# Optimization experiments

Hardware: AMD Instinct MI355X
Metric: run time of the kernel (lower is better)

## Reference

```python
import jax, jax.numpy as jnp
import numpy as np
from jax import lax

DIM = 512          # model dim
L = 32             # img_size
N = L * L          # tokens
H = 4              # heads
C = DIM // 4       # channels per Res2Net scale
D = C // H         # per-head dim = 32 (== dim_head)
B = 8
SCALE = 32 ** -0.5  # dim_head ** -0.5
EPS = 1e-5


def setup_inputs() -> dict:
    key = jax.random.key(0)
    ks = jax.random.split(key, 13)
    nrm = lambda k, s, std: jax.random.normal(k, s, jnp.float32) * std
    uni = lambda k, s: jax.random.uniform(k, s, jnp.float32, 0.5, 1.5)
    return {
        "x": nrm(ks[0], (B, N, DIM), 1.0),
        "w_in": nrm(ks[1], (DIM, DIM), DIM ** -0.5),
        "bn1_g": uni(ks[2], (DIM,)),
        "bn1_b": nrm(ks[3], (DIM,), 0.1),
        "bn1_m": nrm(ks[4], (DIM,), 0.1),
        "bn1_v": uni(ks[5], (DIM,)),
        "w_dw": nrm(ks[6], (C, 1, 3, 3), 1.0 / 3.0),
        "w_pw": nrm(ks[7], (C, C), C ** -0.5),
        "bn2_g": uni(ks[8], (C,)),
        "bn2_b": nrm(ks[9], (C,), 0.1),
        "bn2_m": nrm(ks[10], (C,), 0.1),
        "bn2_v": uni(ks[11], (C,)),
        "w_out": nrm(ks[12], (DIM, DIM), DIM ** -0.5),
    }


def _bn(x, g, b, m, v):
    # eval-mode BatchNorm2d over NCHW
    inv = g / jnp.sqrt(v + EPS)
    return x * inv[None, :, None, None] + (b - m * inv)[None, :, None, None]


def _forward(x, w_in, bn1_g, bn1_b, bn1_m, bn1_v,
             w_dw, w_pw, bn2_g, bn2_b, bn2_m, bn2_v, w_out):
    b = x.shape[0]
    # 'b (l w) n -> b n l w'
    xi = x.transpose(0, 2, 1).reshape(b, DIM, L, L)
    # Res2Net: inconv (1x1 conv + BN)
    ident = jnp.einsum('oc,bchw->bohw', w_in, xi)
    ident = _bn(ident, bn1_g, bn1_b, bn1_m, bn1_v)
    xs = jnp.split(ident, 4, axis=1)

    def x3conv(t):
        t = lax.conv_general_dilated(
            t, w_dw, window_strides=(1, 1), padding='SAME',
            feature_group_count=C,
            dimension_numbers=('NCHW', 'OIHW', 'NCHW'))
        t = jnp.einsum('oc,bchw->bohw', w_pw, t)
        return _bn(t, bn2_g, bn2_b, bn2_m, bn2_v)

    ys = [xs[0]]
    ys.append(x3conv(xs[1]))
    ys.append(x3conv(xs[2] + ys[1]))
    ys.append(x3conv(xs[3] + ys[2]))
    y = jnp.stack(ys, axis=1)  # [b, 4, C, L, L]

    # 'b (h d) l w -> b h (l w) d' per scale; batch the 4 scales together
    qkv = y.reshape(b, 4, H, D, N).transpose(0, 1, 2, 4, 3)  # [b,4,h,n,d]
    att = jnp.einsum('bshid,bshjd->bshij', qkv, qkv) * SCALE   # [b,4,h,n,n]
    att = jax.nn.softmax(att, axis=-1)
    o = jnp.einsum('bshij,bshjd->bshid', att, qkv)             # [b,4,h,n,d]
    # cat over scales of 'b h n d -> b n (h d)' => [b, n, (s h d)] = [b, n, DIM]
    o = o.transpose(0, 3, 1, 2, 4).reshape(b, N, DIM)
    return o @ w_out.T  # Linear(dim, dim, bias=False); dropout is identity (eval)


def reference(x, w_in, bn1_g, bn1_b, bn1_m, bn1_v,
              w_dw, w_pw, bn2_g, bn2_b, bn2_m, bn2_v, w_out):
    return _forward(x, w_in, bn1_g, bn1_b, bn1_m, bn1_v,
                    w_dw, w_pw, bn2_g, bn2_b, bn2_m, bn2_v, w_out)
```

## Files before the change

kernel.cpp:

```cpp
#include <hip/hip_runtime.h>
#include <hip/hip_bf16.h>


#define DIMM 512
#define NTOK 1024
#define CC   128
#define DD   32
#define BB   8
#define EPSB 1e-5f
#define SCALE_ATT 0.17677669529663687f
#define K2EXP (SCALE_ATT * 1.4426950408889634f)
#define TJ 128

typedef __attribute__((ext_vector_type(8))) short short8;
typedef __attribute__((ext_vector_type(4))) float f32x4;

__device__ __forceinline__ unsigned short f2bf(float f) {
    unsigned int x = __float_as_uint(f);
    unsigned int r = x + 0x7fffu + ((x >> 16) & 1u);
    return (unsigned short)(r >> 16);
}
__device__ __forceinline__ unsigned int f2bf2(float lo, float hi) {
    return (unsigned int)f2bf(lo) | ((unsigned int)f2bf(hi) << 16);
}
__device__ __forceinline__ void gl_lds16(const void* g, void* l) {
    __builtin_amdgcn_global_load_lds(
        (const __attribute__((address_space(1))) unsigned int*)g,
        (__attribute__((address_space(3))) unsigned int*)l, 16, 0, 0);
}

__global__ __launch_bounds__(256) void k_mm_in(
    const float* __restrict__ w_in,
    const float* __restrict__ x,
    const float* __restrict__ g1, const float* __restrict__ b1,
    const float* __restrict__ m1, const float* __restrict__ v1,
    float* __restrict__ Y)
{
    __shared__ __align__(16) unsigned short As[128][72];
    __shared__ __align__(16) unsigned short Bs[128][72];
    const int r0 = blockIdx.x * 128;
    const int o0 = blockIdx.y * 128;
    const int b  = r0 >> 10, nloc0 = r0 & 1023;
    const int t = threadIdx.x, wid = t >> 6, lane = t & 63;
    const int l16 = lane & 15, quad = lane >> 4;
    const int wm = (wid >> 1) * 64, wn = (wid & 1) * 64;

    f32x4 acc[4][4];
#pragma unroll
    for (int i = 0; i < 4; i++)
#pragma unroll
        for (int j = 0; j < 4; j++) acc[i][j] = (f32x4){0.f, 0.f, 0.f, 0.f};

    for (int k0 = 0; k0 < DIMM; k0 += 64) {
        __syncthreads();
#pragma unroll
        for (int it = 0; it < 8; it++) {
            int flat = it * 256 + t;
            int row = flat >> 4, c4 = flat & 15;
            float4 w4 = *(const float4*)&w_in[(size_t)(o0 + row) * DIMM + k0 + c4 * 4];
            *(uint2*)&As[row][c4 * 4] = make_uint2(f2bf2(w4.x, w4.y), f2bf2(w4.z, w4.w));
            float4 x4 = *(const float4*)&x[(size_t)(r0 + row) * DIMM + k0 + c4 * 4];
            *(uint2*)&Bs[row][c4 * 4] = make_uint2(f2bf2(x4.x, x4.y), f2bf2(x4.z, x4.w));
        }
        __syncthreads();
#pragma unroll
        for (int kk = 0; kk < 2; kk++) {
            short8 af[4], bf_[4];
#pragma unroll
            for (int i = 0; i < 4; i++) af[i]  = *(const short8*)&As[wm + i * 16 + l16][kk * 32 + quad * 8];
#pragma unroll
            for (int j = 0; j < 4; j++) bf_[j] = *(const short8*)&Bs[wn + j * 16 + l16][kk * 32 + quad * 8];
#pragma unroll
            for (int i = 0; i < 4; i++)
#pragma unroll
                for (int j = 0; j < 4; j++)
                    acc[i][j] = __builtin_amdgcn_mfma_f32_16x16x32_bf16(af[i], bf_[j], acc[i][j], 0, 0, 0);
        }
    }
#pragma unroll
    for (int i = 0; i < 4; i++)
#pragma unroll
        for (int r = 0; r < 4; r++) {
            int o = o0 + wm + i * 16 + quad * 4 + r;
            float inv  = g1[o] / sqrtf(v1[o] + EPSB);
            float beta = b1[o] - m1[o] * inv;
#pragma unroll
            for (int j = 0; j < 4; j++) {
                int n = nloc0 + wn + j * 16 + l16;
                Y[((size_t)b * DIMM + o) * NTOK + n] = acc[i][j][r] * inv + beta;
            }
        }
}

__global__ __launch_bounds__(256) void k_dwconv(
    const float* __restrict__ Y, const float* __restrict__ w_dw,
    float* __restrict__ tmp, int s)
{
    __shared__ float img[34][34];
    const int c = blockIdx.x;
    const int b = blockIdx.y;
    const int t = threadIdx.x;
    for (int i = t; i < 34 * 34; i += 256) (&img[0][0])[i] = 0.f;
    __syncthreads();
    const float* src0 = Y + ((size_t)b * DIMM + s * CC + c) * NTOK;
    const float* src1 = (s >= 2) ? (Y + ((size_t)b * DIMM + (s - 1) * CC + c) * NTOK) : nullptr;
    for (int p = t; p < NTOK; p += 256) {
        float v = src0[p];
        if (src1) v += src1[p];
        img[(p >> 5) + 1][(p & 31) + 1] = v;
    }
    __syncthreads();
    float w[9];
#pragma unroll
    for (int i = 0; i < 9; i++) w[i] = w_dw[c * 9 + i];
    for (int p = t; p < NTOK; p += 256) {
        int yy = p >> 5, xx = p & 31;
        float s0 = 0.f;
#pragma unroll
        for (int ky = 0; ky < 3; ky++)
#pragma unroll
            for (int kx = 0; kx < 3; kx++)
                s0 += img[yy + ky][xx + kx] * w[ky * 3 + kx];
        tmp[((size_t)b * CC + c) * NTOK + p] = s0;
    }
}

__global__ __launch_bounds__(256) void k_mm_pw(
    const float* __restrict__ tmp, const float* __restrict__ w_pw,
    const float* __restrict__ g2, const float* __restrict__ b2,
    const float* __restrict__ m2, const float* __restrict__ v2,
    float* __restrict__ Y, int s)
{
    __shared__ __align__(16) unsigned short As[128][72];
    __shared__ __align__(16) unsigned short Bs[64][72];
    const int n0 = blockIdx.x * 64;
    const int b  = blockIdx.y;
    const int t = threadIdx.x, wid = t >> 6, lane = t & 63;
    const int l16 = lane & 15, quad = lane >> 4;
    const int wm = (wid >> 1) * 64, wn = (wid & 1) * 32;

    f32x4 acc[4][2];
#pragma unroll
    for (int i = 0; i < 4; i++) { acc[i][0] = (f32x4){0.f,0.f,0.f,0.f}; acc[i][1] = (f32x4){0.f,0.f,0.f,0.f}; }

    for (int k0 = 0; k0 < CC; k0 += 64) {
        __syncthreads();
#pragma unroll
        for (int it = 0; it < 8; it++) {
            int flat = it * 256 + t;
            int row = flat >> 4, c4 = flat & 15;
            float4 w4 = *(const float4*)&w_pw[(size_t)row * CC + k0 + c4 * 4];
            *(uint2*)&As[row][c4 * 4] = make_uint2(f2bf2(w4.x, w4.y), f2bf2(w4.z, w4.w));
        }
#pragma unroll
        for (int it = 0; it < 4; it++) {
            int flat = it * 256 + t;
            int c = flat >> 4, n4 = (flat & 15) * 4;
            float4 v = *(const float4*)&tmp[((size_t)b * CC + k0 + c) * NTOK + n0 + n4];
            Bs[n4 + 0][c] = f2bf(v.x);
            Bs[n4 + 1][c] = f2bf(v.y);
            Bs[n4 + 2][c] = f2bf(v.z);
            Bs[n4 + 3][c] = f2bf(v.w);
        }
        __syncthreads();
#pragma unroll
        for (int kk = 0; kk < 2; kk++) {
            short8 af[4], bf_[2];
#pragma unroll
            for (int i = 0; i < 4; i++) af[i]  = *(const short8*)&As[wm + i * 16 + l16][kk * 32 + quad * 8];
#pragma unroll
            for (int j = 0; j < 2; j++) bf_[j] = *(const short8*)&Bs[wn + j * 16 + l16][kk * 32 + quad * 8];
#pragma unroll
            for (int i = 0; i < 4; i++)
#pragma unroll
                for (int j = 0; j < 2; j++)
                    acc[i][j] = __builtin_amdgcn_mfma_f32_16x16x32_bf16(af[i], bf_[j], acc[i][j], 0, 0, 0);
        }
    }
#pragma unroll
    for (int i = 0; i < 4; i++)
#pragma unroll
        for (int r = 0; r < 4; r++) {
            int o = wm + i * 16 + quad * 4 + r;
            float inv  = g2[o] / sqrtf(v2[o] + EPSB);
            float beta = b2[o] - m2[o] * inv;
#pragma unroll
            for (int j = 0; j < 2; j++) {
                int n = n0 + wn + j * 16 + l16;
                Y[((size_t)b * DIMM + s * CC + o) * NTOK + n] = acc[i][j][r] * inv + beta;
            }
        }
}

__global__ __launch_bounds__(256) void k_prep(
    const float* __restrict__ Y,
    unsigned short* __restrict__ Vp,
    unsigned short* __restrict__ Qt)
{
    __shared__ float T[32][129];
    const int jt = blockIdx.x;
    const int n0 = jt * 128;
    const int g  = blockIdx.y;
    const int b = g >> 4, s = (g >> 2) & 3, h = g & 3;
    const int cb = s * CC + h * DD;
    const int t = threadIdx.x;
#pragma unroll
    for (int k = 0; k < 8; k++) {
        int idx = k * 256 + t;
        int d = idx >> 6, jp = (idx & 63) * 2;
        float2 v = *(const float2*)&Y[((size_t)b * DIMM + cb + d) * NTOK + n0 + jp];
        T[d][jp] = v.x; T[d][jp + 1] = v.y;
    }
    __syncthreads();
#pragma unroll
    for (int k = 0; k < 8; k++) {
        int idx = k * 256 + t;
        int n = idx >> 4, dp = (idx & 15) * 2;
        *(unsigned int*)&Qt[((size_t)g * NTOK + n0 + n) * DD + dp] = f2bf2(T[dp][n], T[dp + 1][n]);
    }
#pragma unroll
    for (int e2 = 0; e2 < 2; e2++) {
        int e = e2 * 256 + t;
        int sub = e >> 6, lane = e & 63;
        int quad = lane >> 4, l16 = lane & 15;
        int d  = (sub & 1) * 16 + l16;
        int jb = (sub >> 1) * 32 + quad * 4;
        uint4 v;
        v.x = f2bf2(T[d][jb + 0],  T[d][jb + 1]);
        v.y = f2bf2(T[d][jb + 2],  T[d][jb + 3]);
        v.z = f2bf2(T[d][jb + 16], T[d][jb + 17]);
        v.w = f2bf2(T[d][jb + 18], T[d][jb + 19]);
        *(uint4*)&Vp[((((size_t)g * 8 + jt) * 8 + sub) * 64 + lane) * 8] = v;
    }
}

__global__ __launch_bounds__(256) void k_attn(
    const unsigned short* __restrict__ Qtg,
    const unsigned short* __restrict__ Vp,
    unsigned short* __restrict__ Ob)
{
    __shared__ __align__(16) unsigned short Kt[2][128][32];
    __shared__ __align__(16) unsigned short Vt[2][8][64][8];

    const int blk = blockIdx.x;
    const int g = blk & 127, ib = blk >> 7;
    const int b = g >> 4;
    const int s = (g >> 2) & 3, h = g & 3;
    const int cb = s * CC + h * DD;
    const unsigned short* Qt = Qtg + (size_t)g * NTOK * DD;
    const unsigned short* Vg = Vp + (size_t)g * 8 * 8 * 64 * 8;
    const int t = threadIdx.x;
    const int wid = t >> 6, lane = t & 63;
    const int l16 = lane & 15, quad = lane >> 4;
    const int i0 = ib * 128 + wid * 16 + l16;
    const int i1 = i0 + 64;

    const short8 qi0 = *(const short8*)&Qt[(size_t)i0 * DD + quad * 8];
    const short8 qi1 = *(const short8*)&Qt[(size_t)i1 * DD + quad * 8];
    const short8 ones = {0x3F80, 0x3F80, 0x3F80, 0x3F80, 0x3F80, 0x3F80, 0x3F80, 0x3F80};

    const int krow_l = lane >> 2;
    const int kgcol  = ((lane & 3) ^ ((lane >> 3) & 3)) * 8;
    const int kswz = (quad ^ ((l16 >> 1) & 3)) * 8;

    float dq0 = 0.f, dq1 = 0.f;
#pragma unroll
    for (int e = 0; e < 8; e++) {
        float v0 = __uint_as_float(((unsigned int)(unsigned short)qi0[e]) << 16);
        float v1 = __uint_as_float(((unsigned int)(unsigned short)qi1[e]) << 16);
        dq0 = fmaf(v0, v0, dq0);
        dq1 = fmaf(v1, v1, dq1);
    }
    dq0 += __shfl_xor(dq0, 16); dq0 += __shfl_xor(dq0, 32);
    dq1 += __shfl_xor(dq1, 16); dq1 += __shfl_xor(dq1, 32);
    const float mnk0 = dq0 * K2EXP;
    const float mnk1 = dq1 * K2EXP;

    f32x4 lacc0 = {0.f,0.f,0.f,0.f}, lacc1 = {0.f,0.f,0.f,0.f};
    f32x4 oacc0[2] = {{0.f,0.f,0.f,0.f},{0.f,0.f,0.f,0.f}};
    f32x4 oacc1[2] = {{0.f,0.f,0.f,0.f},{0.f,0.f,0.f,0.f}};
    const f32x4 zero4 = {0.f, 0.f, 0.f, 0.f};

    auto stage = [&](int bsel, int jt_) {
#pragma unroll
        for (int c = 0; c < 2; c++) {
            int grow = jt_ * TJ + wid * 32 + c * 16 + krow_l;
            gl_lds16(&Qt[(size_t)grow * DD + kgcol], &Kt[bsel][wid * 32 + c * 16][0]);
        }
#pragma unroll
        for (int c = 0; c < 2; c++) {
            int sub = wid * 2 + c;
            gl_lds16(&Vg[(((size_t)jt_ * 8 + sub) * 64 + lane) * 8], &Vt[bsel][sub][0][0]);
        }
    };

    stage(0, 0);
    __syncthreads();

    for (int jt = 0; jt < 8; jt++) {
        const int cur = jt & 1;
        if (jt < 7) stage(cur ^ 1, jt + 1);

        short8 pb0[4], pb1[4];
#pragma unroll
        for (int jb = 0; jb < 8; jb++) {
            short8 qj = *(const short8*)&Kt[cur][jb * 16 + l16][kswz];
            f32x4 s0 = __builtin_amdgcn_mfma_f32_16x16x32_bf16(qj, qi0, zero4, 0, 0, 0);
            f32x4 s1 = __builtin_amdgcn_mfma_f32_16x16x32_bf16(qj, qi1, zero4, 0, 0, 0);
            float a0 = __builtin_amdgcn_exp2f(fmaf(s0[0], K2EXP, -mnk0));
            float a1 = __builtin_amdgcn_exp2f(fmaf(s0[1], K2EXP, -mnk0));
            float a2 = __builtin_amdgcn_exp2f(fmaf(s0[2], K2EXP, -mnk0));
            float a3 = __builtin_amdgcn_exp2f(fmaf(s0[3], K2EXP, -mnk0));
            ((unsigned int*)&pb0[jb >> 1])[(jb & 1) * 2] =
                __builtin_amdgcn_perm(__float_as_uint(a1), __float_as_uint(a0), 0x07060302u);
            ((unsigned int*)&pb0[jb >> 1])[(jb & 1) * 2 + 1] =
                __builtin_amdgcn_perm(__float_as_uint(a3), __float_as_uint(a2), 0x07060302u);
            float c0 = __builtin_amdgcn_exp2f(fmaf(s1[0], K2EXP, -mnk1));
            float c1 = __builtin_amdgcn_exp2f(fmaf(s1[1], K2EXP, -mnk1));
            float c2 = __builtin_amdgcn_exp2f(fmaf(s1[2], K2EXP, -mnk1));
            float c3 = __builtin_amdgcn_exp2f(fmaf(s1[3], K2EXP, -mnk1));
            ((unsigned int*)&pb1[jb >> 1])[(jb & 1) * 2] =
                __builtin_amdgcn_perm(__float_as_uint(c1), __float_as_uint(c0), 0x07060302u);
            ((unsigned int*)&pb1[jb >> 1])[(jb & 1) * 2 + 1] =
                __builtin_amdgcn_perm(__float_as_uint(c3), __float_as_uint(c2), 0x07060302u);
        }

#pragma unroll
        for (int wp = 0; wp < 4; wp++) {
            short8 af0 = *(const short8*)&Vt[cur][wp * 2 + 0][lane][0];
            short8 af1 = *(const short8*)&Vt[cur][wp * 2 + 1][lane][0];
            oacc0[0] = __builtin_amdgcn_mfma_f32_16x16x32_bf16(af0, pb0[wp], oacc0[0], 0, 0, 0);
            oacc0[1] = __builtin_amdgcn_mfma_f32_16x16x32_bf16(af1, pb0[wp], oacc0[1], 0, 0, 0);
            lacc0    = __builtin_amdgcn_mfma_f32_16x16x32_bf16(ones, pb0[wp], lacc0, 0, 0, 0);
            oacc1[0] = __builtin_amdgcn_mfma_f32_16x16x32_bf16(af0, pb1[wp], oacc1[0], 0, 0, 0);
            oacc1[1] = __builtin_amdgcn_mfma_f32_16x16x32_bf16(af1, pb1[wp], oacc1[1], 0, 0, 0);
            lacc1    = __builtin_amdgcn_mfma_f32_16x16x32_bf16(ones, pb1[wp], lacc1, 0, 0, 0);
        }

        __syncthreads();
    }

    float invl0 = 1.f / lacc0[0];
    float invl1 = 1.f / lacc1[0];
#pragma unroll
    for (int dblk = 0; dblk < 2; dblk++) {
        uint2 pkd;
        pkd.x = f2bf2(oacc0[dblk][0] * invl0, oacc0[dblk][1] * invl0);
        pkd.y = f2bf2(oacc0[dblk][2] * invl0, oacc0[dblk][3] * invl0);
        *(uint2*)&Ob[((size_t)b * NTOK + i0) * DIMM + cb + dblk * 16 + quad * 4] = pkd;
        pkd.x = f2bf2(oacc1[dblk][0] * invl1, oacc1[dblk][1] * invl1);
        pkd.y = f2bf2(oacc1[dblk][2] * invl1, oacc1[dblk][3] * invl1);
        *(uint2*)&Ob[((size_t)b * NTOK + i1) * DIMM + cb + dblk * 16 + quad * 4] = pkd;
    }
}

__global__ __launch_bounds__(256) void k_mm_out(
    const unsigned short* __restrict__ Oin,
    const float* __restrict__ w_out,
    float* __restrict__ out)
{
    __shared__ __align__(16) unsigned short As[128][72];
    __shared__ __align__(16) unsigned short Bs[128][72];
    const int r0 = blockIdx.x * 128;
    const int o0 = blockIdx.y * 128;
    const int t = threadIdx.x, wid = t >> 6, lane = t & 63;
    const int l16 = lane & 15, quad = lane >> 4;
    const int wm = (wid >> 1) * 64, wn = (wid & 1) * 64;

    f32x4 acc[4][4];
#pragma unroll
    for (int i = 0; i < 4; i++)
#pragma unroll
        for (int j = 0; j < 4; j++) acc[i][j] = (f32x4){0.f, 0.f, 0.f, 0.f};

    for (int k0 = 0; k0 < DIMM; k0 += 64) {
        __syncthreads();
#pragma unroll
        for (int q = 0; q < 4; q++) {
            int flat = q * 256 + t;
            int row = flat >> 3, c8 = flat & 7;
            *(short8*)&As[row][c8 * 8] = *(const short8*)&Oin[(size_t)(r0 + row) * DIMM + k0 + c8 * 8];
        }
#pragma unroll
        for (int it = 0; it < 8; it++) {
            int flat = it * 256 + t;
            int row = flat >> 4, c4 = flat & 15;
            float4 w4 = *(const float4*)&w_out[(size_t)(o0 + row) * DIMM + k0 + c4 * 4];
            *(uint2*)&Bs[row][c4 * 4] = make_uint2(f2bf2(w4.x, w4.y), f2bf2(w4.z, w4.w));
        }
        __syncthreads();
#pragma unroll
        for (int kk = 0; kk < 2; kk++) {
            short8 af[4], bf_[4];
#pragma unroll
            for (int i = 0; i < 4; i++) af[i]  = *(const short8*)&As[wm + i * 16 + l16][kk * 32 + quad * 8];
#pragma unroll
            for (int j = 0; j < 4; j++) bf_[j] = *(const short8*)&Bs[wn + j * 16 + l16][kk * 32 + quad * 8];
#pragma unroll
            for (int i = 0; i < 4; i++)
#pragma unroll
                for (int j = 0; j < 4; j++)
                    acc[i][j] = __builtin_amdgcn_mfma_f32_16x16x32_bf16(af[i], bf_[j], acc[i][j], 0, 0, 0);
        }
    }
#pragma unroll
    for (int i = 0; i < 4; i++)
#pragma unroll
        for (int r = 0; r < 4; r++) {
            int rr = r0 + wm + i * 16 + quad * 4 + r;
#pragma unroll
            for (int j = 0; j < 4; j++) {
                int o = o0 + wn + j * 16 + l16;
                out[(size_t)rr * DIMM + o] = acc[i][j][r];
            }
        }
}

extern "C" void kernel_launch(void* const* d_in, const int* in_sizes, int n_in,
                              void* d_out, int out_size, void* d_ws, size_t ws_size,
                              hipStream_t stream)
{
    const float* x    = (const float*)d_in[0];
    const float* w_in = (const float*)d_in[1];
    const float* g1   = (const float*)d_in[2];
    const float* b1   = (const float*)d_in[3];
    const float* m1   = (const float*)d_in[4];
    const float* v1   = (const float*)d_in[5];
    const float* wdw  = (const float*)d_in[6];
    const float* wpw  = (const float*)d_in[7];
    const float* g2   = (const float*)d_in[8];
    const float* b2   = (const float*)d_in[9];
    const float* m2   = (const float*)d_in[10];
    const float* v2   = (const float*)d_in[11];
    const float* wout = (const float*)d_in[12];
    float* out = (float*)d_out;

    char* base = (char*)d_ws;
    float*          Y   = (float*)base;
    unsigned short* Ob  = (unsigned short*)base;
    float*          tmp = (float*)(base + (size_t)16 * 1024 * 1024);
    unsigned short* Vp  = (unsigned short*)(base + (size_t)16 * 1024 * 1024);
    unsigned short* Qt  = (unsigned short*)(base + (size_t)24 * 1024 * 1024);

    k_mm_in<<<dim3(64, 4), 256, 0, stream>>>(w_in, x, g1, b1, m1, v1, Y);
    for (int s = 1; s <= 3; s++) {
        k_dwconv<<<dim3(CC, BB), 256, 0, stream>>>(Y, wdw, tmp, s);
        k_mm_pw<<<dim3(16, 8), 256, 0, stream>>>(tmp, wpw, g2, b2, m2, v2, Y, s);
    }
    k_prep<<<dim3(8, 128), 256, 0, stream>>>(Y, Vp, Qt);
    k_attn<<<dim3(1024), 256, 0, stream>>>(Qt, Vp, Ob);
    k_mm_out<<<dim3(64, 4), 256, 0, stream>>>(Ob, wout, out);
}
```

Before: 194.2 us.

## Fuse Q/V bf16 packing into GEMM epilogues and store dwconv output as bf16

The separate k_prep kernel is removed. Its transpose-and-pack work producing the Qt and Vp bf16 layouts now runs in the epilogues of k_mm_in (scale 0 only) and k_mm_pw, staged through reused shared memory. k_dwconv writes bf16 instead of fp32, halving its traffic and dropping the conversion in k_mm_pw's loads. The last scale skips writing Y, and workspace buffers are reshuffled to alias free regions. In exchange, the epilogues get extra barriers and more work, and the buffer aliasing is delicate.

```diff
diff --git a/kernel.cpp b/kernel.cpp
--- a/kernel.cpp
+++ b/kernel.cpp
@@ -13,6 +13,7 @@
 #define TJ 128
 
 typedef __attribute__((ext_vector_type(8))) short short8;
+typedef __attribute__((ext_vector_type(4))) short short4v;
 typedef __attribute__((ext_vector_type(4))) float f32x4;
 
 __device__ __forceinline__ unsigned short f2bf(float f) {
@@ -34,10 +35,15 @@
     const float* __restrict__ x,
     const float* __restrict__ g1, const float* __restrict__ b1,
     const float* __restrict__ m1, const float* __restrict__ v1,
-    float* __restrict__ Y)
+    float* __restrict__ Y,
+    unsigned short* __restrict__ Vp,
+    unsigned short* __restrict__ Qt)
 {
-    __shared__ __align__(16) unsigned short As[128][72];
-    __shared__ __align__(16) unsigned short Bs[128][72];
+    __shared__ __align__(16) unsigned short SM[2][128][72];
+    unsigned short (*As)[72] = SM[0];
+    unsigned short (*Bs)[72] = SM[1];
+    unsigned short (*Tn)[144] = (unsigned short (*)[144])&SM[0][0][0];
+
     const int r0 = blockIdx.x * 128;
     const int o0 = blockIdx.y * 128;
     const int b  = r0 >> 10, nloc0 = r0 & 1023;
@@ -77,24 +83,77 @@
                     acc[i][j] = __builtin_amdgcn_mfma_f32_16x16x32_bf16(af[i], bf_[j], acc[i][j], 0, 0, 0);
         }
     }
-#pragma unroll
-    for (int i = 0; i < 4; i++)
-#pragma unroll
-        for (int r = 0; r < 4; r++) {
-            int o = o0 + wm + i * 16 + quad * 4 + r;
-            float inv  = g1[o] / sqrtf(v1[o] + EPSB);
-            float beta = b1[o] - m1[o] * inv;
-#pragma unroll
-            for (int j = 0; j < 4; j++) {
-                int n = nloc0 + wn + j * 16 + l16;
-                Y[((size_t)b * DIMM + o) * NTOK + n] = acc[i][j][r] * inv + beta;
+
+    if (o0 == 0) {
+        __syncthreads();
+#pragma unroll
+        for (int i = 0; i < 4; i++)
+#pragma unroll
+            for (int r = 0; r < 4; r++) {
+                int ol = wm + i * 16 + quad * 4 + r;
+                float inv  = g1[ol] / sqrtf(v1[ol] + EPSB);
+                float beta = b1[ol] - m1[ol] * inv;
+#pragma unroll
+                for (int j = 0; j < 4; j++) {
+                    int nn = wn + j * 16 + l16;
+                    float val = acc[i][j][r] * inv + beta;
+                    Y[((size_t)b * DIMM + ol) * NTOK + nloc0 + nn] = val;
+                    Tn[ol][nn] = f2bf(val);
+                }
             }
-        }
+        __syncthreads();
+        const int jt = nloc0 >> 7;
+#pragma unroll
+        for (int it = 0; it < 2; it++) {
+            int idx = it * 256 + t;
+            int nl = idx & 127, h = idx >> 7;
+            int g = b * 16 + h;
+            unsigned int w[16];
+#pragma unroll
+            for (int dp = 0; dp < 16; dp++)
+                w[dp] = (unsigned int)Tn[h * 32 + dp * 2][nl] | ((unsigned int)Tn[h * 32 + dp * 2 + 1][nl] << 16);
+            unsigned short* qdst = &Qt[((size_t)g * NTOK + nloc0 + nl) * DD];
+            ((uint4*)qdst)[0] = make_uint4(w[0],  w[1],  w[2],  w[3]);
+            ((uint4*)qdst)[1] = make_uint4(w[4],  w[5],  w[6],  w[7]);
+            ((uint4*)qdst)[2] = make_uint4(w[8],  w[9],  w[10], w[11]);
+            ((uint4*)qdst)[3] = make_uint4(w[12], w[13], w[14], w[15]);
+        }
+#pragma unroll
+        for (int it = 0; it < 8; it++) {
+            int slot = it * 256 + t;
+            int h = slot >> 9, rest = slot & 511;
+            int sub = rest >> 6, lp = rest & 63;
+            int d  = (sub & 1) * 16 + (lp & 15);
+            int jb = (sub >> 1) * 32 + (lp >> 4) * 4;
+            int ol = h * 32 + d;
+            int g = b * 16 + h;
+            uint4 v;
+            v.x = (unsigned int)Tn[ol][jb + 0]  | ((unsigned int)Tn[ol][jb + 1]  << 16);
+            v.y = (unsigned int)Tn[ol][jb + 2]  | ((unsigned int)Tn[ol][jb + 3]  << 16);
+            v.z = (unsigned int)Tn[ol][jb + 16] | ((unsigned int)Tn[ol][jb + 17] << 16);
+            v.w = (unsigned int)Tn[ol][jb + 18] | ((unsigned int)Tn[ol][jb + 19] << 16);
+            *(uint4*)&Vp[((((size_t)g * 8 + jt) * 8 + sub) * 64 + lp) * 8] = v;
+        }
+    } else {
+#pragma unroll
+        for (int i = 0; i < 4; i++)
+#pragma unroll
+            for (int r = 0; r < 4; r++) {
+                int o = o0 + wm + i * 16 + quad * 4 + r;
+                float inv  = g1[o] / sqrtf(v1[o] + EPSB);
+                float beta = b1[o] - m1[o] * inv;
+#pragma unroll
+                for (int j = 0; j < 4; j++) {
+                    int n = nloc0 + wn + j * 16 + l16;
+                    Y[((size_t)b * DIMM + o) * NTOK + n] = acc[i][j][r] * inv + beta;
+                }
+            }
+    }
 }
 
 __global__ __launch_bounds__(256) void k_dwconv(
     const float* __restrict__ Y, const float* __restrict__ w_dw,
-    float* __restrict__ tmp, int s)
+    unsigned short* __restrict__ tmpb, long long bstride, int s)
 {
     __shared__ float img[34][34];
     const int c = blockIdx.x;
@@ -113,6 +172,7 @@
     float w[9];
 #pragma unroll
     for (int i = 0; i < 9; i++) w[i] = w_dw[c * 9 + i];
+    unsigned short* dst = tmpb + (size_t)b * bstride + (size_t)c * NTOK;
     for (int p = t; p < NTOK; p += 256) {
         int yy = p >> 5, xx = p & 31;
         float s0 = 0.f;
@@ -121,15 +181,18 @@
 #pragma unroll
             for (int kx = 0; kx < 3; kx++)
                 s0 += img[yy + ky][xx + kx] * w[ky * 3 + kx];
-        tmp[((size_t)b * CC + c) * NTOK + p] = s0;
+        dst[p] = f2bf(s0);
     }
 }
 
 __global__ __launch_bounds__(256) void k_mm_pw(
-    const float* __restrict__ tmp, const float* __restrict__ w_pw,
+    const unsigned short* __restrict__ tmpb, long long bstride,
+    const float* __restrict__ w_pw,
     const float* __restrict__ g2, const float* __restrict__ b2,
     const float* __restrict__ m2, const float* __restrict__ v2,
-    float* __restrict__ Y, int s)
+    float* __restrict__ Y,
+    unsigned short* __restrict__ Vp,
+    unsigned short* __restrict__ Qt, int s)
 {
     __shared__ __align__(16) unsigned short As[128][72];
     __shared__ __align__(16) unsigned short Bs[64][72];
@@ -143,6 +206,7 @@
 #pragma unroll
     for (int i = 0; i < 4; i++) { acc[i][0] = (f32x4){0.f,0.f,0.f,0.f}; acc[i][1] = (f32x4){0.f,0.f,0.f,0.f}; }
 
+    const unsigned short* tb = tmpb + (size_t)b * bstride;
     for (int k0 = 0; k0 < CC; k0 += 64) {
         __syncthreads();
 #pragma unroll
@@ -156,11 +220,11 @@
         for (int it = 0; it < 4; it++) {
             int flat = it * 256 + t;
             int c = flat >> 4, n4 = (flat & 15) * 4;
-            float4 v = *(const float4*)&tmp[((size_t)b * CC + k0 + c) * NTOK + n0 + n4];
-            Bs[n4 + 0][c] = f2bf(v.x);
-            Bs[n4 + 1][c] = f2bf(v.y);
-            Bs[n4 + 2][c] = f2bf(v.z);
-            Bs[n4 + 3][c] = f2bf(v.w);
+            short4v v = *(const short4v*)&tb[(size_t)(k0 + c) * NTOK + n0 + n4];
+            Bs[n4 + 0][c] = (unsigned short)v[0];
+            Bs[n4 + 1][c] = (unsigned short)v[1];
+            Bs[n4 + 2][c] = (unsigned short)v[2];
+            Bs[n4 + 3][c] = (unsigned short)v[3];
         }
         __syncthreads();
 #pragma unroll
@@ -177,60 +241,57 @@
                     acc[i][j] = __builtin_amdgcn_mfma_f32_16x16x32_bf16(af[i], bf_[j], acc[i][j], 0, 0, 0);
         }
     }
+
+    __syncthreads();
 #pragma unroll
     for (int i = 0; i < 4; i++)
 #pragma unroll
         for (int r = 0; r < 4; r++) {
-            int o = wm + i * 16 + quad * 4 + r;
-            float inv  = g2[o] / sqrtf(v2[o] + EPSB);
-            float beta = b2[o] - m2[o] * inv;
+            int ol = wm + i * 16 + quad * 4 + r;
+            float inv  = g2[ol] / sqrtf(v2[ol] + EPSB);
+            float beta = b2[ol] - m2[ol] * inv;
 #pragma unroll
             for (int j = 0; j < 2; j++) {
-                int n = n0 + wn + j * 16 + l16;
-                Y[((size_t)b * DIMM + s * CC + o) * NTOK + n] = acc[i][j][r] * inv + beta;
+                int nn = wn + j * 16 + l16;
+                float val = acc[i][j][r] * inv + beta;
+                if (s < 3) Y[((size_t)b * DIMM + s * CC + ol) * NTOK + n0 + nn] = val;
+                As[ol][nn] = f2bf(val);
             }
         }
-}
-
-__global__ __launch_bounds__(256) void k_prep(
-    const float* __restrict__ Y,
-    unsigned short* __restrict__ Vp,
-    unsigned short* __restrict__ Qt)
-{
-    __shared__ float T[32][129];
-    const int jt = blockIdx.x;
-    const int n0 = jt * 128;
-    const int g  = blockIdx.y;
-    const int b = g >> 4, s = (g >> 2) & 3, h = g & 3;
-    const int cb = s * CC + h * DD;
-    const int t = threadIdx.x;
-#pragma unroll
-    for (int k = 0; k < 8; k++) {
-        int idx = k * 256 + t;
-        int d = idx >> 6, jp = (idx & 63) * 2;
-        float2 v = *(const float2*)&Y[((size_t)b * DIMM + cb + d) * NTOK + n0 + jp];
-        T[d][jp] = v.x; T[d][jp + 1] = v.y;
-    }
     __syncthreads();
-#pragma unroll
-    for (int k = 0; k < 8; k++) {
-        int idx = k * 256 + t;
-        int n = idx >> 4, dp = (idx & 15) * 2;
-        *(unsigned int*)&Qt[((size_t)g * NTOK + n0 + n) * DD + dp] = f2bf2(T[dp][n], T[dp + 1][n]);
-    }
-#pragma unroll
-    for (int e2 = 0; e2 < 2; e2++) {
-        int e = e2 * 256 + t;
-        int sub = e >> 6, lane = e & 63;
-        int quad = lane >> 4, l16 = lane & 15;
-        int d  = (sub & 1) * 16 + l16;
-        int jb = (sub >> 1) * 32 + quad * 4;
+
+    const int jt = n0 >> 7;
+    const int n0l = n0 & 127;
+    {
+        int nl = t & 63, h = t >> 6;
+        int g = b * 16 + s * 4 + h;
+        unsigned int w[16];
+#pragma unroll
+        for (int dp = 0; dp < 16; dp++)
+            w[dp] = (unsigned int)As[h * 32 + dp * 2][nl] | ((unsigned int)As[h * 32 + dp * 2 + 1][nl] << 16);
+        unsigned short* qdst = &Qt[((size_t)g * NTOK + n0 + nl) * DD];
+        ((uint4*)qdst)[0] = make_uint4(w[0],  w[1],  w[2],  w[3]);
+        ((uint4*)qdst)[1] = make_uint4(w[4],  w[5],  w[6],  w[7]);
+        ((uint4*)qdst)[2] = make_uint4(w[8],  w[9],  w[10], w[11]);
+        ((uint4*)qdst)[3] = make_uint4(w[12], w[13], w[14], w[15]);
+    }
+#pragma unroll
+    for (int it = 0; it < 4; it++) {
+        int slot = it * 256 + t;
+        int h = slot >> 8, rest = slot & 255;
+        int sl = rest >> 6, lp = rest & 63;
+        int dhi = sl & 1, sbo = sl >> 1;
+        int sub = ((n0l >> 5) + sbo) * 2 + dhi;
+        int d = dhi * 16 + (lp & 15);
+        int ol = h * 32 + d;
+        int jbl = sbo * 32 + (lp >> 4) * 4;
+        int g = b * 16 + s * 4 + h;
         uint4 v;
-        v.x = f2bf2(T[d][jb + 0],  T[d][jb + 1]);
-        v.y = f2bf2(T[d][jb + 2],  T[d][jb + 3]);
-        v.z = f2bf2(T[d][jb + 16], T[d][jb + 17]);
-        v.w = f2bf2(T[d][jb + 18], T[d][jb + 19]);
-        *(uint4*)&Vp[((((size_t)g * 8 + jt) * 8 + sub) * 64 + lane) * 8] = v;
+        v.x = (unsigned int)As[ol][jbl + 0]  | ((unsigned int)As[ol][jbl + 1]  << 16);
+        v.y = (unsigned int)As[ol][jbl + 2]  | ((unsigned int)As[ol][jbl + 3]  << 16);
+        v.z = (unsigned int)As[ol][jbl + 16] | ((unsigned int)As[ol][jbl + 17] << 16);
+        v.w = (unsigned int)As[ol][jbl + 18] | ((unsigned int)As[ol][jbl + 19] << 16);
+        *(uint4*)&Vp[((((size_t)g * 8 + jt) * 8 + sub) * 64 + lp) * 8] = v;
     }
 }
 
@@ -438,16 +499,25 @@
     char* base = (char*)d_ws;
     float*          Y   = (float*)base;
     unsigned short* Ob  = (unsigned short*)base;
-    float*          tmp = (float*)(base + (size_t)16 * 1024 * 1024);
-    unsigned short* Vp  = (unsigned short*)(base + (size_t)16 * 1024 * 1024);
-    unsigned short* Qt  = (unsigned short*)(base + (size_t)24 * 1024 * 1024);
-
-    k_mm_in<<<dim3(64, 4), 256, 0, stream>>>(w_in, x, g1, b1, m1, v1, Y);
-    for (int s = 1; s <= 3; s++) {
-        k_dwconv<<<dim3(CC, BB), 256, 0, stream>>>(Y, wdw, tmp, s);
-        k_mm_pw<<<dim3(16, 8), 256, 0, stream>>>(tmp, wpw, g2, b2, m2, v2, Y, s);
-    }
-    k_prep<<<dim3(8, 128), 256, 0, stream>>>(Y, Vp, Qt);
+    unsigned short* Qt  = (unsigned short*)(base + (size_t)16 * 1024 * 1024);
+    unsigned short* Vp  = (unsigned short*)(base + (size_t)24 * 1024 * 1024);
+
+    unsigned short* tmp1 = Qt + (size_t)12 * NTOK * DD;
+    const long long  bstride1 = (long long)16 * NTOK * DD;
+    unsigned short* tmp23 = (unsigned short*)Y;
+    const long long  bstride23 = (long long)DIMM * NTOK * 2;
+
+    k_mm_in<<<dim3(64, 4), 256, 0, stream>>>(w_in, x, g1, b1, m1, v1, Y, Vp, Qt);
+
+    k_dwconv<<<dim3(CC, BB), 256, 0, stream>>>(Y, wdw, tmp1, bstride1, 1);
+    k_mm_pw<<<dim3(16, 8), 256, 0, stream>>>(tmp1, bstride1, wpw, g2, b2, m2, v2, Y, Vp, Qt, 1);
+
+    k_dwconv<<<dim3(CC, BB), 256, 0, stream>>>(Y, wdw, tmp23, bstride23, 2);
+    k_mm_pw<<<dim3(16, 8), 256, 0, stream>>>(tmp23, bstride23, wpw, g2, b2, m2, v2, Y, Vp, Qt, 2);
+
+    k_dwconv<<<dim3(CC, BB), 256, 0, stream>>>(Y, wdw, tmp23, bstride23, 3);
+    k_mm_pw<<<dim3(16, 8), 256, 0, stream>>>(tmp23, bstride23, wpw, g2, b2, m2, v2, Y, Vp, Qt, 3);
+
     k_attn<<<dim3(1024), 256, 0, stream>>>(Qt, Vp, Ob);
     k_mm_out<<<dim3(64, 4), 256, 0, stream>>>(Ob, wout, out);
 }
```

After: 195.1 us. No clear change (+0.4%).
